# Kernel tuning notes

Hardware: AMD Instinct MI355X
Metric: run time of the kernel (lower is better)

## Reference

```python
import jax, jax.numpy as jnp
import numpy as np

KH = KW = 3
STRIDE = 2
PAD = 1


def _extract_patches(x, kh, kw, stride, pad):
    # x: [B, C, H, W] -> patches [B, C, Ho, Wo, kh*kw]
    B, C, H, W = x.shape
    xp = jnp.pad(x, ((0, 0), (0, 0), (pad, pad), (pad, pad)))
    Ho = (H + 2 * pad - kh) // stride + 1
    Wo = (W + 2 * pad - kw) // stride + 1
    cols = [
        xp[:, :, i : i + stride * Ho : stride, j : j + stride * Wo : stride]
        for i in range(kh)
        for j in range(kw)
    ]
    return jnp.stack(cols, axis=-1)  # [B, C, Ho, Wo, kh*kw]


def setup_inputs() -> dict:
    key = jax.random.key(0)
    k1, k2 = jax.random.split(key)
    x = jax.random.normal(k1, (32, 64, 112, 112), dtype=jnp.float32)
    s = jax.random.normal(k2, (64, KH, KW), dtype=jnp.float32) * 0.1
    return {"x": x, "s": s}


def reference(x, s):
    # RRSVM rank-weighted pooling: for each sliding window, sort values
    # descending and take a weighted sum with per-channel rank weights s.
    patches = _extract_patches(x, KH, KW, STRIDE, PAD)  # [B,C,Ho,Wo,K]
    order = jnp.argsort(-patches, axis=-1)              # descending ranks
    sorted_vals = jnp.take_along_axis(patches, order, axis=-1)
    s_flat = s.reshape(s.shape[0], KH * KW)             # [C, K]
    out = jnp.einsum("bchwk,ck->bchw", sorted_vals, s_flat)
    return out, order.astype(jnp.int64)
```

## Files before the change

### kernel.cpp

```cpp
#include <hip/hip_runtime.h>


constexpr int B  = 32;
constexpr int C  = 64;
constexpr int H  = 112;
constexpr int W  = 112;
constexpr int HO = 56;
constexpr int WO = 56;
constexpr int KK = 9;
constexpr int NPIX = HO * WO;
constexpr int BLK  = 256;

__global__ __launch_bounds__(BLK) void rrsvm_kernel(
    const float* __restrict__ x, const float* __restrict__ s,
    float* __restrict__ out, float* __restrict__ order)
{
    __shared__ float lorder[BLK * KK];

    const int plane = blockIdx.y;
    const int tid   = threadIdx.x;
    const int pix0  = blockIdx.x * BLK;
    const int pix   = pix0 + tid;
    const bool live = (pix < NPIX);
    const int ho = pix / WO;
    const int wo = pix - ho * WO;
    const int c  = plane & (C - 1);

    const float* xp = x + (size_t)plane * (H * W);

    float v[KK];
    int   id[KK];
    const int iy0 = 2 * ho - 1;
    const int ix0 = 2 * wo - 1;
#pragma unroll
    for (int dy = 0; dy < 3; ++dy) {
        const int  iy  = iy0 + dy;
        const bool yok = live && ((unsigned)iy < (unsigned)H);
#pragma unroll
        for (int dx = 0; dx < 3; ++dx) {
            const int  ix = ix0 + dx;
            const int  k  = dy * 3 + dx;
            const bool ok = yok && ((unsigned)ix < (unsigned)W);
            v[k]  = ok ? xp[iy * W + ix] : 0.0f;
            id[k] = k;
        }
    }

    auto CE = [&](int a, int b) {
        const float va = v[a],  vb = v[b];
        const int   ia = id[a], ib = id[b];
        const bool sw = (va < vb) || ((va == vb) && (ia > ib));
        v[a]  = sw ? vb : va;  v[b]  = sw ? va : vb;
        id[a] = sw ? ib : ia;  id[b] = sw ? ia : ib;
    };

    CE(0,1); CE(2,3); CE(4,5); CE(6,7);
    CE(0,2); CE(1,3); CE(4,6); CE(5,7);
    CE(1,2); CE(5,6);
    CE(0,4); CE(1,5); CE(2,6); CE(3,7);
    CE(2,4); CE(3,5);
    CE(1,2); CE(3,4); CE(5,6);
    CE(7,8); CE(6,7); CE(5,6); CE(4,5); CE(3,4); CE(2,3); CE(1,2); CE(0,1);

    const float* sc = s + c * KK;
    float acc = 0.0f;
#pragma unroll
    for (int k = 0; k < KK; ++k) acc = fmaf(v[k], sc[k], acc);

    if (live) out[(size_t)plane * NPIX + pix] = acc;

#pragma unroll
    for (int k = 0; k < KK; ++k) lorder[tid * KK + k] = (float)id[k];
    __syncthreads();

    const int nwin = min(BLK, NPIX - pix0);
    const int nf4  = (nwin * KK) >> 2;
    float4* __restrict__ ob =
        (float4*)(order + ((size_t)plane * NPIX + pix0) * KK);
    const float4* __restrict__ lb = (const float4*)lorder;
    for (int i = tid; i < nf4; i += BLK) ob[i] = lb[i];
}

extern "C" void kernel_launch(void* const* d_in, const int* in_sizes, int n_in,
                              void* d_out, int out_size, void* d_ws, size_t ws_size,
                              hipStream_t stream) {
    const float* x = (const float*)d_in[0];
    const float* s = (const float*)d_in[1];
    float* out   = (float*)d_out;
    float* order = out + (size_t)B * C * NPIX;

    dim3 grid((NPIX + BLK - 1) / BLK, B * C);
    rrsvm_kernel<<<grid, dim3(BLK), 0, stream>>>(x, s, out, order);
}
```

Measured before the change: 328.0 us.

## Stage input rows in shared memory and map waves to output rows

Each block now loads nine input rows of a plane with coalesced float4 reads into LDS, with zero padding at the left border and at rows outside the image. Each of four waves then computes one output row by reading its 3x3 windows from LDS instead of issuing strided global loads. This is meant to cut redundant, uncoalesced global traffic for overlapping windows. In exchange, each wave has 8 idle lanes, the kernel adds a barrier, and the stride-2 LDS accesses may cause bank conflicts.

```diff
diff --git a/kernel.cpp b/kernel.cpp
--- a/kernel.cpp
+++ b/kernel.cpp
@@ -10,41 +10,53 @@
 constexpr int KK = 9;
 constexpr int NPIX = HO * WO;
 constexpr int BLK  = 256;
+constexpr int LROW = 128;
+constexpr int RPT  = 4;
+constexpr int IR   = 2 * RPT + 1;
 
 __global__ __launch_bounds__(BLK) void rrsvm_kernel(
     const float* __restrict__ x, const float* __restrict__ s,
     float* __restrict__ out, float* __restrict__ order)
 {
-    __shared__ float lorder[BLK * KK];
+    __shared__ float lx[IR * LROW];
+    __shared__ float lorder[RPT * WO * KK];
 
     const int plane = blockIdx.y;
+    const int ho0   = blockIdx.x;
     const int tid   = threadIdx.x;
-    const int pix0  = blockIdx.x * BLK;
-    const int pix   = pix0 + tid;
-    const bool live = (pix < NPIX);
-    const int ho = pix / WO;
-    const int wo = pix - ho * WO;
-    const int c  = plane & (C - 1);
+    const int w     = tid >> 6;
+    const int lane  = tid & 63;
+    const int c     = plane & (C - 1);
 
     const float* xp = x + (size_t)plane * (H * W);
 
+    if (tid < IR * (W / 4)) {
+        const int r = tid / (W / 4);
+        const int cc = tid - r * (W / 4);
+        const int grow = 8 * ho0 - 1 + r;
+        float4 val = make_float4(0.f, 0.f, 0.f, 0.f);
+        if ((unsigned)grow < (unsigned)H)
+            val = *(const float4*)(xp + grow * W + 4 * cc);
+        float* dst = &lx[r * LROW + 1 + 4 * cc];
+        dst[0] = val.x; dst[1] = val.y; dst[2] = val.z; dst[3] = val.w;
+    }
+    if (tid < IR) lx[tid * LROW] = 0.0f;
+    __syncthreads();
+
+    const bool live = (lane < WO);
+    const int  lc   = live ? lane : 0;
+    const int  ho   = ho0 * RPT + w;
+
     float v[KK];
     int   id[KK];
-    const int iy0 = 2 * ho - 1;
-    const int ix0 = 2 * wo - 1;
 #pragma unroll
-    for (int dy = 0; dy < 3; ++dy) {
-        const int  iy  = iy0 + dy;
-        const bool yok = live && ((unsigned)iy < (unsigned)H);
+    for (int dy = 0; dy < 3; ++dy)
 #pragma unroll
         for (int dx = 0; dx < 3; ++dx) {
-            const int  ix = ix0 + dx;
-            const int  k  = dy * 3 + dx;
-            const bool ok = yok && ((unsigned)ix < (unsigned)W);
-            v[k]  = ok ? xp[iy * W + ix] : 0.0f;
+            const int k = dy * 3 + dx;
+            v[k]  = lx[(2 * w + dy) * LROW + 2 * lc + dx];
             id[k] = k;
         }
-    }
 
     auto CE = [&](int a, int b) {
         const float va = v[a],  vb = v[b];
@@ -53,7 +65,6 @@
         v[a]  = sw ? vb : va;  v[b]  = sw ? va : vb;
         id[a] = sw ? ib : ia;  id[b] = sw ? ia : ib;
     };
-
     CE(0,1); CE(2,3); CE(4,5); CE(6,7);
     CE(0,2); CE(1,3); CE(4,6); CE(5,7);
     CE(1,2); CE(5,6);
@@ -67,18 +78,21 @@
 #pragma unroll
     for (int k = 0; k < KK; ++k) acc = fmaf(v[k], sc[k], acc);
 
-    if (live) out[(size_t)plane * NPIX + pix] = acc;
-
+    if (live) {
+        out[(size_t)plane * NPIX + ho * WO + lane] = acc;
+        const int widx = w * WO + lane;
 #pragma unroll
-    for (int k = 0; k < KK; ++k) lorder[tid * KK + k] = (float)id[k];
+        for (int k = 0; k < KK; ++k)
+            lorder[widx * KK + k] = (float)id[k];
+    }
     __syncthreads();
 
-    const int nwin = min(BLK, NPIX - pix0);
-    const int nf4  = (nwin * KK) >> 2;
     float4* __restrict__ ob =
-        (float4*)(order + ((size_t)plane * NPIX + pix0) * KK);
+        (float4*)(order + ((size_t)plane * NPIX + (size_t)ho0 * RPT * WO) * KK);
     const float4* __restrict__ lb = (const float4*)lorder;
-    for (int i = tid; i < nf4; i += BLK) ob[i] = lb[i];
+#pragma unroll
+    for (int i = tid; i < RPT * WO * KK / 4; i += BLK)
+        ob[i] = lb[i];
 }
 
 extern "C" void kernel_launch(void* const* d_in, const int* in_sizes, int n_in,
@@ -89,6 +103,6 @@
     float* out   = (float*)d_out;
     float* order = out + (size_t)B * C * NPIX;
 
-    dim3 grid((NPIX + BLK - 1) / BLK, B * C);
+    dim3 grid(HO / RPT, B * C);
     rrsvm_kernel<<<grid, dim3(BLK), 0, stream>>>(x, s, out, order);
 }
```

After: 323.7 us. No clear change (-1.3%).
